# Kernel optimization log

Hardware: AMD Instinct MI355X
Metric: run time of the kernel (lower is better)

The kernel has to match this reference:

```python
import jax, jax.numpy as jnp
import numpy as np

D = 2048
N_EXPERTS = 64
K = 2


def setup_inputs() -> dict:
    key = jax.random.key(0)
    kx, kw = jax.random.split(key)
    x = jax.random.normal(kx, (4, 4096, D), dtype=jnp.float32)
    # xavier_uniform for Linear(d, n_experts): bound = sqrt(6/(fan_in+fan_out))
    bound = float(np.sqrt(6.0 / (D + N_EXPERTS)))
    W = jax.random.uniform(kw, (N_EXPERTS, D), dtype=jnp.float32, minval=-bound, maxval=bound)
    b = jnp.zeros((N_EXPERTS,), dtype=jnp.float32)
    return {"x": x, "W": W, "b": b}


def reference(x, W, b):
    # logits: [B, S, E]  (eval mode: no noise)
    logits = jnp.einsum("bsd,ed->bse", x, W) + b
    topk_vals, topk_idx = jax.lax.top_k(logits, K)  # [B, S, K]
    gates = jax.nn.softmax(topk_vals, axis=-1)
    return gates, topk_idx
```

## Files before the change

kernel.cpp:

```cpp
#include <hip/hip_runtime.h>
#include <math.h>

#define DD 2048
#define EE 64
#define TM 32
#define BK 64
#define NCHUNK (DD / BK)
#define THREADS 256

#define ROWB 144
#define XPLANE (TM * ROWB)
#define WPLANE (EE * ROWB)
#define BUFB   (2 * XPLANE + 2 * WPLANE)

typedef _Float16 f16x8 __attribute__((ext_vector_type(8)));
typedef _Float16 f16x4 __attribute__((ext_vector_type(4)));
typedef float    f32x4 __attribute__((ext_vector_type(4)));

__device__ static inline void split_f4(const float4 v, f16x4& hi, f16x4& lo) {
    const float S = 32.f;
    const float a0 = v.x * S, a1 = v.y * S, a2 = v.z * S, a3 = v.w * S;
    const _Float16 h0 = (_Float16)a0, h1 = (_Float16)a1;
    const _Float16 h2 = (_Float16)a2, h3 = (_Float16)a3;
    hi = (f16x4){h0, h1, h2, h3};
    lo = (f16x4){(_Float16)(a0 - (float)h0), (_Float16)(a1 - (float)h1),
                 (_Float16)(a2 - (float)h2), (_Float16)(a3 - (float)h3)};
}

__global__ __launch_bounds__(THREADS) void router_kernel(
    const float* __restrict__ x, const float* __restrict__ W,
    const float* __restrict__ bias_g, float* __restrict__ out, int n_tokens)
{
    __shared__ __attribute__((aligned(16))) char  lds[2 * BUFB];
    __shared__ __attribute__((aligned(16))) float logits[TM * (EE + 1)];

    const int tid   = threadIdx.x;
    const int tBase = blockIdx.x * TM;

    const int xt = tid >> 3;
    const int xc = tid & 7;
    const int we = tid >> 2;
    const int wc = tid & 3;

    const float* xrow = x + (size_t)(tBase + xt) * DD + xc * 4;
    const float* wrow = W + (size_t)we * DD + wc * 4;

    float4 rx[2], rw[4];

#define LOADX(c) { _Pragma("unroll") for (int p = 0; p < 2; ++p) \
        rx[p] = *(const float4*)&xrow[(c) * BK + p * 32]; }
#define LOADW(c) { _Pragma("unroll") for (int q = 0; q < 4; ++q) \
        rw[q] = *(const float4*)&wrow[(c) * BK + q * 16]; }

#define WRITE_STAGE(buf) { \
    char* base = lds + (buf) * BUFB; \
    char* xh = base; char* xl = base + XPLANE; \
    char* wh = base + 2 * XPLANE; char* wl = base + 2 * XPLANE + WPLANE; \
    _Pragma("unroll") for (int p = 0; p < 2; ++p) { \
        f16x4 hi, lo; split_f4(rx[p], hi, lo); \
        const int off = xt * ROWB + (xc + 8 * p) * 8; \
        *(f16x4*)(xh + off) = hi; *(f16x4*)(xl + off) = lo; \
    } \
    _Pragma("unroll") for (int q = 0; q < 4; ++q) { \
        f16x4 hi, lo; split_f4(rw[q], hi, lo); \
        const int off = we * ROWB + (wc + 4 * q) * 8; \
        *(f16x4*)(wh + off) = hi; *(f16x4*)(wl + off) = lo; \
    } }

    const int wv   = tid >> 6;
    const int lane = tid & 63;
    const int mtile = wv & 1;
    const int ngrp  = wv >> 1;
    const int r16  = lane & 15;
    const int kg   = lane >> 4;

    const int aoff  = (mtile * 16 + r16) * ROWB + kg * 16;
    const int boff0 = ((ngrp * 2 + 0) * 16 + r16) * ROWB + kg * 16;
    const int boff1 = ((ngrp * 2 + 1) * 16 + r16) * ROWB + kg * 16;

    f32x4 acc0 = {0.f, 0.f, 0.f, 0.f};
    f32x4 acc1 = {0.f, 0.f, 0.f, 0.f};

#define COMPUTE(buf) { \
    char* base = lds + (buf) * BUFB; \
    char* xh = base; char* xl = base + XPLANE; \
    char* wh = base + 2 * XPLANE; char* wl = base + 2 * XPLANE + WPLANE; \
    _Pragma("unroll") for (int ks = 0; ks < 2; ++ks) { \
        const int ko = ks * 64; \
        const f16x8 ah  = *(const f16x8*)(xh + aoff  + ko); \
        const f16x8 al  = *(const f16x8*)(xl + aoff  + ko); \
        const f16x8 bh0 = *(const f16x8*)(wh + boff0 + ko); \
        const f16x8 bl0 = *(const f16x8*)(wl + boff0 + ko); \
        const f16x8 bh1 = *(const f16x8*)(wh + boff1 + ko); \
        const f16x8 bl1 = *(const f16x8*)(wl + boff1 + ko); \
        acc0 = __builtin_amdgcn_mfma_f32_16x16x32_f16(ah, bh0, acc0, 0, 0, 0); \
        acc0 = __builtin_amdgcn_mfma_f32_16x16x32_f16(al, bh0, acc0, 0, 0, 0); \
        acc0 = __builtin_amdgcn_mfma_f32_16x16x32_f16(ah, bl0, acc0, 0, 0, 0); \
        acc0 = __builtin_amdgcn_mfma_f32_16x16x32_f16(al, bl0, acc0, 0, 0, 0); \
        acc1 = __builtin_amdgcn_mfma_f32_16x16x32_f16(ah, bh1, acc1, 0, 0, 0); \
        acc1 = __builtin_amdgcn_mfma_f32_16x16x32_f16(al, bh1, acc1, 0, 0, 0); \
        acc1 = __builtin_amdgcn_mfma_f32_16x16x32_f16(ah, bl1, acc1, 0, 0, 0); \
        acc1 = __builtin_amdgcn_mfma_f32_16x16x32_f16(al, bl1, acc1, 0, 0, 0); \
    } }

    LOADX(0); LOADW(0);
    WRITE_STAGE(0);
    LOADX(1); LOADW(1);

    int cur = 0;
    for (int c = 0; c < NCHUNK; ++c) {
        __syncthreads();
        COMPUTE(cur);
        if (c + 1 < NCHUNK) {
            WRITE_STAGE(cur ^ 1);
            if (c + 2 < NCHUNK) { LOADX(c + 2); LOADW(c + 2); }
        }
        cur ^= 1;
    }

    const int col0 = ngrp * 32 + r16;
    const int col1 = ngrp * 32 + 16 + r16;
    const float b0 = bias_g[col0];
    const float b1 = bias_g[col1];
    const float INV = 1.f / 1024.f;
    const int rbase = mtile * 16 + kg * 4;
#pragma unroll
    for (int r = 0; r < 4; ++r) {
        logits[(rbase + r) * (EE + 1) + col0] = acc0[r] * INV + b0;
        logits[(rbase + r) * (EE + 1) + col1] = acc1[r] * INV + b1;
    }
    __syncthreads();

    if (tid < TM) {
        const float* lrow = &logits[tid * (EE + 1)];
        float v1 = -INFINITY, v2 = -INFINITY;
        int   i1 = 0, i2 = 0;
        for (int e = 0; e < EE; ++e) {
            const float v = lrow[e];
            if (v > v1) { v2 = v1; i2 = i1; v1 = v; i1 = e; }
            else if (v > v2) { v2 = v; i2 = e; }
        }
        const float ed = expf(v2 - v1);
        const float inv = 1.f / (1.f + ed);
        const int tok = tBase + tid;
        out[tok * 2 + 0] = inv;
        out[tok * 2 + 1] = ed * inv;
        float* oidx = out + (size_t)2 * n_tokens;
        oidx[tok * 2 + 0] = (float)i1;
        oidx[tok * 2 + 1] = (float)i2;
    }
}

extern "C" void kernel_launch(void* const* d_in, const int* in_sizes, int n_in,
                              void* d_out, int out_size, void* d_ws, size_t ws_size,
                              hipStream_t stream) {
    const float* x = (const float*)d_in[0];
    const float* W = (const float*)d_in[1];
    const float* b = (const float*)d_in[2];
    float* out = (float*)d_out;

    const int n_tokens = in_sizes[0] / DD;
    const int n_blocks = n_tokens / TM;

    router_kernel<<<n_blocks, THREADS, 0, stream>>>(x, W, b, out, n_tokens);
}
```

Before: 203.2 us.

## Double threads, interleave hi/lo fp16 planes, and drop lo*lo MFMA term

```diff
diff --git a/kernel.cpp b/kernel.cpp
--- a/kernel.cpp
+++ b/kernel.cpp
@@ -6,28 +6,30 @@
 #define TM 32
 #define BK 64
 #define NCHUNK (DD / BK)
-#define THREADS 256
+#define THREADS 512
 
-#define ROWB 144
+#define ROWB 272
 #define XPLANE (TM * ROWB)
 #define WPLANE (EE * ROWB)
-#define BUFB   (2 * XPLANE + 2 * WPLANE)
+#define BUFB   (XPLANE + WPLANE)
 
 typedef _Float16 f16x8 __attribute__((ext_vector_type(8)));
-typedef _Float16 f16x4 __attribute__((ext_vector_type(4)));
 typedef float    f32x4 __attribute__((ext_vector_type(4)));
 
-__device__ static inline void split_f4(const float4 v, f16x4& hi, f16x4& lo) {
+__device__ static inline void split8(const float4 a, const float4 b,
+                                     f16x8& hi, f16x8& lo) {
     const float S = 32.f;
-    const float a0 = v.x * S, a1 = v.y * S, a2 = v.z * S, a3 = v.w * S;
-    const _Float16 h0 = (_Float16)a0, h1 = (_Float16)a1;
-    const _Float16 h2 = (_Float16)a2, h3 = (_Float16)a3;
-    hi = (f16x4){h0, h1, h2, h3};
-    lo = (f16x4){(_Float16)(a0 - (float)h0), (_Float16)(a1 - (float)h1),
-                 (_Float16)(a2 - (float)h2), (_Float16)(a3 - (float)h3)};
+    const float v[8] = {a.x * S, a.y * S, a.z * S, a.w * S,
+                        b.x * S, b.y * S, b.z * S, b.w * S};
+#pragma unroll
+    for (int i = 0; i < 8; ++i) {
+        const _Float16 h = (_Float16)v[i];
+        hi[i] = h;
+        lo[i] = (_Float16)(v[i] - (float)h);
+    }
 }
 
-__global__ __launch_bounds__(THREADS) void router_kernel(
+__global__ __launch_bounds__(THREADS, 4) void router_kernel(
     const float* __restrict__ x, const float* __restrict__ W,
     const float* __restrict__ bias_g, float* __restrict__ out, int n_tokens)
 {
@@ -37,70 +39,55 @@
     const int tid   = threadIdx.x;
     const int tBase = blockIdx.x * TM;
 
-    const int xt = tid >> 3;
-    const int xc = tid & 7;
-    const int we = tid >> 2;
-    const int wc = tid & 3;
+    const int sr = tid >> 3;
+    const int sg = tid & 7;
+    const bool do_x = (sr < TM);
 
-    const float* xrow = x + (size_t)(tBase + xt) * DD + xc * 4;
-    const float* wrow = W + (size_t)we * DD + wc * 4;
+    const float* xrow = x + (size_t)(tBase + (sr & (TM - 1))) * DD + sg * 8;
+    const float* wrow = W + (size_t)sr * DD + sg * 8;
 
-    float4 rx[2], rw[4];
+    float4 rx0 = {0,0,0,0}, rx1 = {0,0,0,0}, rw0, rw1;
 
-#define LOADX(c) { _Pragma("unroll") for (int p = 0; p < 2; ++p) \
-        rx[p] = *(const float4*)&xrow[(c) * BK + p * 32]; }
-#define LOADW(c) { _Pragma("unroll") for (int q = 0; q < 4; ++q) \
-        rw[q] = *(const float4*)&wrow[(c) * BK + q * 16]; }
+#define LOADX(c) { if (do_x) { \
+        rx0 = *(const float4*)&xrow[(c) * BK];     \
+        rx1 = *(const float4*)&xrow[(c) * BK + 4]; } }
+#define LOADW(c) { \
+        rw0 = *(const float4*)&wrow[(c) * BK];     \
+        rw1 = *(const float4*)&wrow[(c) * BK + 4]; }
 
 #define WRITE_STAGE(buf) { \
-    char* base = lds + (buf) * BUFB; \
-    char* xh = base; char* xl = base + XPLANE; \
-    char* wh = base + 2 * XPLANE; char* wl = base + 2 * XPLANE + WPLANE; \
-    _Pragma("unroll") for (int p = 0; p < 2; ++p) { \
-        f16x4 hi, lo; split_f4(rx[p], hi, lo); \
-        const int off = xt * ROWB + (xc + 8 * p) * 8; \
-        *(f16x4*)(xh + off) = hi; *(f16x4*)(xl + off) = lo; \
-    } \
-    _Pragma("unroll") for (int q = 0; q < 4; ++q) { \
-        f16x4 hi, lo; split_f4(rw[q], hi, lo); \
-        const int off = we * ROWB + (wc + 4 * q) * 8; \
-        *(f16x4*)(wh + off) = hi; *(f16x4*)(wl + off) = lo; \
-    } }
+    char* base = lds + (size_t)(buf) * BUFB; \
+    { f16x8 hi, lo; split8(rw0, rw1, hi, lo); \
+      const int off = XPLANE + sr * ROWB + sg * 32; \
+      *(f16x8*)(base + off)      = hi; \
+      *(f16x8*)(base + off + 16) = lo; } \
+    if (do_x) { f16x8 hi, lo; split8(rx0, rx1, hi, lo); \
+      const int off = sr * ROWB + sg * 32; \
+      *(f16x8*)(base + off)      = hi; \
+      *(f16x8*)(base + off + 16) = lo; } }
 
     const int wv   = tid >> 6;
     const int lane = tid & 63;
-    const int mtile = wv & 1;
-    const int ngrp  = wv >> 1;
+    const int mt   = wv & 1;
+    const int nt   = wv >> 1;
     const int r16  = lane & 15;
     const int kg   = lane >> 4;
 
-    const int aoff  = (mtile * 16 + r16) * ROWB + kg * 16;
-    const int boff0 = ((ngrp * 2 + 0) * 16 + r16) * ROWB + kg * 16;
-    const int boff1 = ((ngrp * 2 + 1) * 16 + r16) * ROWB + kg * 16;
+    const int aoff = (mt * 16 + r16) * ROWB + kg * 32;
+    const int boff = XPLANE + (nt * 16 + r16) * ROWB + kg * 32;
 
-    f32x4 acc0 = {0.f, 0.f, 0.f, 0.f};
-    f32x4 acc1 = {0.f, 0.f, 0.f, 0.f};
+    f32x4 acc = {0.f, 0.f, 0.f, 0.f};
 
 #define COMPUTE(buf) { \
-    char* base = lds + (buf) * BUFB; \
-    char* xh = base; char* xl = base + XPLANE; \
-    char* wh = base + 2 * XPLANE; char* wl = base + 2 * XPLANE + WPLANE; \
+    const char* base = lds + (size_t)(buf) * BUFB; \
     _Pragma("unroll") for (int ks = 0; ks < 2; ++ks) { \
-        const int ko = ks * 64; \
-        const f16x8 ah  = *(const f16x8*)(xh + aoff  + ko); \
-        const f16x8 al  = *(const f16x8*)(xl + aoff  + ko); \
-        const f16x8 bh0 = *(const f16x8*)(wh + boff0 + ko); \
-        const f16x8 bl0 = *(const f16x8*)(wl + boff0 + ko); \
-        const f16x8 bh1 = *(const f16x8*)(wh + boff1 + ko); \
-        const f16x8 bl1 = *(const f16x8*)(wl + boff1 + ko); \
-        acc0 = __builtin_amdgcn_mfma_f32_16x16x32_f16(ah, bh0, acc0, 0, 0, 0); \
-        acc0 = __builtin_amdgcn_mfma_f32_16x16x32_f16(al, bh0, acc0, 0, 0, 0); \
-        acc0 = __builtin_amdgcn_mfma_f32_16x16x32_f16(ah, bl0, acc0, 0, 0, 0); \
-        acc0 = __builtin_amdgcn_mfma_f32_16x16x32_f16(al, bl0, acc0, 0, 0, 0); \
-        acc1 = __builtin_amdgcn_mfma_f32_16x16x32_f16(ah, bh1, acc1, 0, 0, 0); \
-        acc1 = __builtin_amdgcn_mfma_f32_16x16x32_f16(al, bh1, acc1, 0, 0, 0); \
-        acc1 = __builtin_amdgcn_mfma_f32_16x16x32_f16(ah, bl1, acc1, 0, 0, 0); \
-        acc1 = __builtin_amdgcn_mfma_f32_16x16x32_f16(al, bl1, acc1, 0, 0, 0); \
+        const f16x8 ah = *(const f16x8*)(base + aoff + ks * 128); \
+        const f16x8 al = *(const f16x8*)(base + aoff + ks * 128 + 16); \
+        const f16x8 bh = *(const f16x8*)(base + boff + ks * 128); \
+        const f16x8 bl = *(const f16x8*)(base + boff + ks * 128 + 16); \
+        acc = __builtin_amdgcn_mfma_f32_16x16x32_f16(ah, bh, acc, 0, 0, 0); \
+        acc = __builtin_amdgcn_mfma_f32_16x16x32_f16(al, bh, acc, 0, 0, 0); \
+        acc = __builtin_amdgcn_mfma_f32_16x16x32_f16(ah, bl, acc, 0, 0, 0); \
     } }
 
     LOADX(0); LOADW(0);
@@ -118,17 +105,14 @@
         cur ^= 1;
     }
 
-    const int col0 = ngrp * 32 + r16;
-    const int col1 = ngrp * 32 + 16 + r16;
-    const float b0 = bias_g[col0];
-    const float b1 = bias_g[col1];
-    const float INV = 1.f / 1024.f;
-    const int rbase = mtile * 16 + kg * 4;
+    __syncthreads();
+    const int col  = nt * 16 + r16;
+    const float bcol = bias_g[col];
+    const float INV  = 1.f / 1024.f;
+    const int rbase  = mt * 16 + kg * 4;
 #pragma unroll
-    for (int r = 0; r < 4; ++r) {
-        logits[(rbase + r) * (EE + 1) + col0] = acc0[r] * INV + b0;
-        logits[(rbase + r) * (EE + 1) + col1] = acc1[r] * INV + b1;
-    }
+    for (int r = 0; r < 4; ++r)
+        logits[(rbase + r) * (EE + 1) + col] = acc[r] * INV + bcol;
     __syncthreads();
 
     if (tid < TM) {
@@ -140,7 +124,7 @@
             if (v > v1) { v2 = v1; i2 = i1; v1 = v; i1 = e; }
             else if (v > v2) { v2 = v; i2 = e; }
         }
-        const float ed = expf(v2 - v1);
+        const float ed  = expf(v2 - v1);
         const float inv = 1.f / (1.f + ed);
         const int tok = tBase + tid;
         out[tok * 2 + 0] = inv;
```

Result: no change. 202.3 us (-0.5%).
